# Kernel tuning notes

Measured on AMD Instinct MI355X. Metric: run time of the kernel, lower is better.

The kernel has to match this reference:

```python
import jax, jax.numpy as jnp
import numpy as np

EMBED_DIM = 768
NUM_HEADS = 12
HEAD_DIM = EMBED_DIM // NUM_HEADS
SCALE = HEAD_DIM ** -0.5


def setup_inputs() -> dict:
    key = jax.random.key(0)
    k_x, k_wqkv, k_bqkv, k_wfc, k_bfc = jax.random.split(key, 5)
    B, S, D = 32, 577, EMBED_DIM
    x = jax.random.normal(k_x, (B, S, D), dtype=jnp.float32)
    # torch Linear default init ~ U(-1/sqrt(fan_in), 1/sqrt(fan_in)); scale suffices
    lim = 1.0 / np.sqrt(D)
    w_qkv = jax.random.uniform(k_wqkv, (D, 3 * D), jnp.float32, -lim, lim)
    b_qkv = jax.random.uniform(k_bqkv, (3 * D,), jnp.float32, -lim, lim)
    w_fc = jax.random.uniform(k_wfc, (D, D), jnp.float32, -lim, lim)
    b_fc = jax.random.uniform(k_bfc, (D,), jnp.float32, -lim, lim)
    return {"x": x, "w_qkv": w_qkv, "b_qkv": b_qkv, "w_fc": w_fc, "b_fc": b_fc}


def reference(x, w_qkv, b_qkv, w_fc, b_fc):
    B, S, D = x.shape
    H, Dh = NUM_HEADS, HEAD_DIM
    qkv = x @ w_qkv + b_qkv                      # [B,S,3D]
    qkv = qkv.reshape(B, S, 3, H, Dh)
    q, k, v = jnp.moveaxis(qkv, 2, 0)            # each [B,S,H,Dh]
    # scores: [B,H,S,S]
    attn = jnp.einsum('bqhd,bkhd->bhqk', q, k) * SCALE
    attn = jax.nn.softmax(attn, axis=-1)
    out = jnp.einsum('bhqk,bkhd->bqhd', attn, v).reshape(B, S, D)
    # dropout in eval mode -> identity
    return out @ w_fc + b_fc
```

## Files before the change

### kernel.cpp

```cpp
#include <hip/hip_runtime.h>
#include <hip/hip_bf16.h>
#include <stdint.h>

typedef __attribute__((ext_vector_type(8))) short short8;
typedef __attribute__((ext_vector_type(4))) float f32x4;

typedef __attribute__((address_space(3))) uint8_t lds_u8;
typedef __attribute__((address_space(1))) uint8_t glb_u8;

__device__ __forceinline__ void load_lds_16(const void* g, void* l) {
    __builtin_amdgcn_global_load_lds((glb_u8*)g, (lds_u8*)l, 16, 0, 0);
}

__device__ __forceinline__ unsigned short f2b(float f) {
    __hip_bfloat16 h = __float2bfloat16(f);
    return __builtin_bit_cast(unsigned short, h);
}
__device__ __forceinline__ ushort2 f2b2(float a, float b) {
    __hip_bfloat162 h = __float22bfloat162_rn(float2{a, b});
    ushort2 r;
    __builtin_memcpy(&r, &h, sizeof(r));
    return r;
}

constexpr int Bz = 32, Ss = 577, Dd = 768, Hh = 12;
constexpr int Mm = Bz * Ss;
constexpr int QKV_N = 3 * Dd;
constexpr float SCALE_L2E = 0.125f * 1.4426950408889634f;

__global__ void cast_f32_bf16(const float* __restrict__ src,
                              unsigned short* __restrict__ dst, int n4) {
    int i = blockIdx.x * blockDim.x + threadIdx.x;
    if (i >= n4) return;
    float4 v = ((const float4*)src)[i];
    ushort4 o;
    o.x = f2b(v.x); o.y = f2b(v.y); o.z = f2b(v.z); o.w = f2b(v.w);
    ((ushort4*)dst)[i] = o;
}

__global__ void transpose_cast(const float* __restrict__ src,
                               unsigned short* __restrict__ dst, int R, int C) {
    __shared__ unsigned short tile[32][33];
    int c0 = blockIdx.x * 32, r0 = blockIdx.y * 32;
    int tx = threadIdx.x, ty = threadIdx.y;
#pragma unroll
    for (int i = 0; i < 4; ++i)
        tile[ty + i * 8][tx] = f2b(src[(size_t)(r0 + ty + i * 8) * C + c0 + tx]);
    __syncthreads();
#pragma unroll
    for (int i = 0; i < 4; ++i) {
        int rr = ty + i * 8;
        dst[(size_t)(c0 + rr) * R + r0 + tx] = tile[tx][rr];
    }
}

template <int N_, bool OUT_BF16>
__global__ __launch_bounds__(256)
void gemm_tn(const unsigned short* __restrict__ A,
             const unsigned short* __restrict__ Bt,
             const float* __restrict__ bias,
             void* __restrict__ Cout) {
    constexpr int K = 768;
    constexpr int KB = K / 32;
    constexpr int NX = N_ / 128;
    constexpr int NY = (Mm + 127) / 128;
    constexpr int NWG = NX * NY;
    constexpr int QC = NWG >> 3, RC = NWG & 7;
    __shared__ __align__(16) uint8_t smem[32768];

    const int tid = threadIdx.x;
    const int wave = tid >> 6, lane = tid & 63;
    const int quad = lane >> 4, lc = lane & 15;
    const int wm = wave >> 1, wn = wave & 1;

    const int orig = blockIdx.y * NX + blockIdx.x;
    const int xcd = orig & 7, lid = orig >> 3;
    const int wgid = (xcd < RC ? xcd * (QC + 1) : RC * (QC + 1) + (xcd - RC) * QC) + lid;
    const int tm = (wgid / NX) * 128;
    const int tn = (wgid % NX) * 128;

    const int l4 = lane >> 2;
    const int cx = (lane & 3) ^ (l4 & 3);

    auto stage = [&](int kb, int buf) {
        uint8_t* Ab = smem + buf * 8192;
        uint8_t* Bb = smem + 16384 + buf * 8192;
#pragma unroll
        for (int i = 0; i < 2; ++i) {
            int lrow = wave * 32 + i * 16 + l4;
            int arow = tm + lrow; if (arow >= Mm) arow = Mm - 1;
            load_lds_16(A + (size_t)arow * K + kb * 32 + cx * 8,
                        (void*)(Ab + (wave * 32 + i * 16) * 64));
            int brow = tn + lrow;
            load_lds_16(Bt + (size_t)brow * K + kb * 32 + cx * 8,
                        (void*)(Bb + (wave * 32 + i * 16) * 64));
        }
    };

    f32x4 acc[4][4] = {};
    stage(0, 0);
    __syncthreads();

    for (int kb = 0; kb < KB; ++kb) {
        const int buf = kb & 1;
        if (kb + 1 < KB) stage(kb + 1, buf ^ 1);

        const unsigned short* Ar = (const unsigned short*)(smem + buf * 8192);
        const unsigned short* Br = (const unsigned short*)(smem + 16384 + buf * 8192);
        short8 af[4], bf[4];
#pragma unroll
        for (int i = 0; i < 4; ++i) {
            int row = wm * 64 + i * 16 + lc;
            int c = quad ^ (row & 3);
            af[i] = *(const short8*)(Ar + row * 32 + c * 8);
            int brow = wn * 64 + i * 16 + lc;
            int cb = quad ^ (brow & 3);
            bf[i] = *(const short8*)(Br + brow * 32 + cb * 8);
        }
#pragma unroll
        for (int i = 0; i < 4; ++i)
#pragma unroll
            for (int j = 0; j < 4; ++j)
                acc[i][j] = __builtin_amdgcn_mfma_f32_16x16x32_bf16(af[i], bf[j], acc[i][j], 0, 0, 0);
        __syncthreads();
    }

    float bv[4];
#pragma unroll
    for (int j = 0; j < 4; ++j) bv[j] = bias[tn + wn * 64 + j * 16 + lc];

    float* ep = (float*)smem + wave * (16 * 68);
    const int erow = lane >> 2, ec = (lane & 3) * 16;
#pragma unroll
    for (int i = 0; i < 4; ++i) {
#pragma unroll
        for (int j = 0; j < 4; ++j)
#pragma unroll
            for (int r = 0; r < 4; ++r)
                ep[(quad * 4 + r) * 68 + j * 16 + lc] = acc[i][j][r] + bv[j];
        __threadfence_block();
        int grow = tm + wm * 64 + i * 16 + erow;
        if (grow < Mm) {
            float4 c0 = *(float4*)&ep[erow * 68 + ec + 0];
            float4 c1 = *(float4*)&ep[erow * 68 + ec + 4];
            float4 c2 = *(float4*)&ep[erow * 68 + ec + 8];
            float4 c3 = *(float4*)&ep[erow * 68 + ec + 12];
            int gcol = tn + wn * 64 + ec;
            if constexpr (OUT_BF16) {
                unsigned short o[16];
                *(ushort2*)&o[0]  = f2b2(c0.x, c0.y);
                *(ushort2*)&o[2]  = f2b2(c0.z, c0.w);
                *(ushort2*)&o[4]  = f2b2(c1.x, c1.y);
                *(ushort2*)&o[6]  = f2b2(c1.z, c1.w);
                *(ushort2*)&o[8]  = f2b2(c2.x, c2.y);
                *(ushort2*)&o[10] = f2b2(c2.z, c2.w);
                *(ushort2*)&o[12] = f2b2(c3.x, c3.y);
                *(ushort2*)&o[14] = f2b2(c3.z, c3.w);
                unsigned short* op = (unsigned short*)Cout + (size_t)grow * N_ + gcol;
                *(short8*)(op + 0) = *(short8*)&o[0];
                *(short8*)(op + 8) = *(short8*)&o[8];
            } else {
                float* op = (float*)Cout + (size_t)grow * N_ + gcol;
                *(float4*)(op + 0)  = c0;
                *(float4*)(op + 4)  = c1;
                *(float4*)(op + 8)  = c2;
                *(float4*)(op + 12) = c3;
            }
        }
        __threadfence_block();
    }
}


template <bool TAIL>
__device__ __forceinline__ void attn_tile(
    const unsigned short* __restrict__ Ktile,
    const unsigned short* __restrict__ Vtb,
    unsigned short* __restrict__ Pqw,
    const short8& qf0, const short8& qf1,
    int quad, int lc,
    f32x4 (&oacc)[4], f32x4& lacc) {

    const int sw = lc & 7;
    f32x4 sfr[4];
#pragma unroll
    for (int f = 0; f < 4; ++f) {
        const unsigned short* kr = Ktile + (f * 16 + lc) * 64;
        short8 k0 = *(const short8*)(kr + (quad ^ sw) * 8);
        short8 k1 = *(const short8*)(kr + ((quad ^ 4) ^ sw) * 8);
        f32x4 z = {};
        z = __builtin_amdgcn_mfma_f32_16x16x32_bf16(k0, qf0, z, 0, 0, 0);
        z = __builtin_amdgcn_mfma_f32_16x16x32_bf16(k1, qf1, z, 0, 0, 0);
        sfr[f] = z;
    }

#pragma unroll
    for (int f = 0; f < 4; ++f) {
        float p[4];
#pragma unroll
        for (int r = 0; r < 4; ++r) {
            float s = sfr[f][r];
            if (TAIL && !(f == 0 && r == 0 && quad == 0)) s = -1e30f;
            p[r] = __builtin_amdgcn_exp2f(s * SCALE_L2E);
        }
        ushort2 lo = f2b2(p[0], p[1]), hi = f2b2(p[2], p[3]);
        ushort4 pk = {lo.x, lo.y, hi.x, hi.y};
        *(ushort4*)&Pqw[lc * 72 + f * 16 + quad * 4] = pk;
    }

    __threadfence_block();

    short8 pf0 = *(const short8*)&Pqw[lc * 72 + quad * 8];
    short8 pf1 = *(const short8*)&Pqw[lc * 72 + 32 + quad * 8];
#pragma unroll
    for (int g = 0; g < 4; ++g) {
        short8 vf0 = *(const short8*)&Vtb[(g * 16 + lc) * 80 + quad * 8];
        short8 vf1 = *(const short8*)&Vtb[(g * 16 + lc) * 80 + 32 + quad * 8];
        oacc[g] = __builtin_amdgcn_mfma_f32_16x16x32_bf16(vf0, pf0, oacc[g], 0, 0, 0);
        oacc[g] = __builtin_amdgcn_mfma_f32_16x16x32_bf16(vf1, pf1, oacc[g], 0, 0, 0);
    }
    short8 vo0 = *(const short8*)&Vtb[(64 + lc) * 80 + quad * 8];
    short8 vo1 = *(const short8*)&Vtb[(64 + lc) * 80 + 32 + quad * 8];
    lacc = __builtin_amdgcn_mfma_f32_16x16x32_bf16(vo0, pf0, lacc, 0, 0, 0);
    lacc = __builtin_amdgcn_mfma_f32_16x16x32_bf16(vo1, pf1, lacc, 0, 0, 0);
}

__global__ __launch_bounds__(512)
void attn_kernel(const unsigned short* __restrict__ qkv,
                 unsigned short* __restrict__ outb) {
    __shared__ unsigned short Kt[2][64 * 64];
    __shared__ unsigned short Vt[2][80 * 80];
    __shared__ unsigned short Pq[8][16 * 72];

    const int tid = threadIdx.x;
    const int wave = tid >> 6, lane = tid & 63;
    const int quad = lane >> 4, lc = lane & 15;

    const int orig = (blockIdx.z * gridDim.y + blockIdx.y) * gridDim.x + blockIdx.x;
    const int wgid = (orig & 7) * 240 + (orig >> 3);
    const int qt = wgid % 5;
    const int h  = (wgid / 5) % Hh;
    const int b  = wgid / (5 * Hh);

    const unsigned short* qkvK = qkv + (size_t)b * Ss * QKV_N + h * 64 + 768;
    const unsigned short* qkvV = qkvK + 768;

    const int krow = lane >> 3;
    const int gch = (lane & 7) ^ krow;

    const int qbase = qt * 128 + wave * 16;
    int qrow = qbase + lc; if (qrow > Ss - 1) qrow = Ss - 1;
    const unsigned short* qp = qkv + (size_t)(b * Ss + qrow) * QKV_N + h * 64;
    short8 qf0 = *(const short8*)(qp + quad * 8);
    short8 qf1 = *(const short8*)(qp + 32 + quad * 8);

    unsigned short* Pqw = Pq[wave];

    auto stage_K = [&](int tile, int buf) {
        int key = tile * 64 + wave * 8 + krow; if (key > Ss - 1) key = Ss - 1;
        const unsigned short* gp = qkvK + (size_t)key * QKV_N + gch * 8;
        load_lds_16(gp, (void*)&Kt[buf][wave * 512]);
    };
    auto load_V = [&](int tile) -> short8 {
        int key = tile * 64 + lane; if (key > Ss - 1) key = Ss - 1;
        return *(const short8*)(qkvV + (size_t)key * QKV_N + wave * 8);
    };
    auto write_V = [&](short8 v, int buf) {
#pragma unroll
        for (int j = 0; j < 8; ++j)
            Vt[buf][(wave * 8 + j) * 80 + lane] = (unsigned short)v[j];
    };

    if (tid < 80) {
        Vt[0][64 * 80 + tid] = 0x3F80;
        Vt[1][64 * 80 + tid] = 0x3F80;
    }

    f32x4 oacc[4] = {};
    f32x4 lacc = {};

    stage_K(0, 0);
    write_V(load_V(0), 0);
    __syncthreads();

    for (int kb = 0; kb < 9; ++kb) {
        const int buf = kb & 1;
        stage_K(kb + 1, buf ^ 1);
        short8 vreg = load_V(kb + 1);
        attn_tile<false>(Kt[buf], Vt[buf], Pqw, qf0, qf1, quad, lc, oacc, lacc);
        write_V(vreg, buf ^ 1);
        __syncthreads();
    }
    attn_tile<true>(Kt[1], Vt[1], Pqw, qf0, qf1, quad, lc, oacc, lacc);

    float lq = __shfl(lacc[0], lc, 64);
    float inv = 1.f / lq;
#pragma unroll
    for (int g = 0; g < 4; ++g) {
        ushort2 lo = f2b2(oacc[g][0] * inv, oacc[g][1] * inv);
        ushort2 hi = f2b2(oacc[g][2] * inv, oacc[g][3] * inv);
        ushort4 ob = {lo.x, lo.y, hi.x, hi.y};
        *(ushort4*)&Pqw[lc * 72 + g * 16 + quad * 4] = ob;
    }
    __threadfence_block();
#pragma unroll
    for (int p = 0; p < 2; ++p) {
        int lr = p * 8 + (lane >> 3), ch = lane & 7;
        int q = qbase + lr;
        if (q <= Ss - 1) {
            short8 vv = *(const short8*)&Pqw[lr * 72 + ch * 8];
            *(short8*)(outb + (size_t)(b * Ss + q) * Dd + h * 64 + ch * 8) = vv;
        }
    }
}

extern "C" void kernel_launch(void* const* d_in, const int* in_sizes, int n_in,
                              void* d_out, int out_size, void* d_ws, size_t ws_size,
                              hipStream_t stream) {
    const float* x     = (const float*)d_in[0];
    const float* w_qkv = (const float*)d_in[1];
    const float* b_qkv = (const float*)d_in[2];
    const float* w_fc  = (const float*)d_in[3];
    const float* b_fc  = (const float*)d_in[4];

    uint8_t* ws = (uint8_t*)d_ws;
    unsigned short* xb    = (unsigned short*)(ws + 0);
    unsigned short* wqkvT = (unsigned short*)(ws + 28360704);
    unsigned short* wfcT  = (unsigned short*)(ws + 31899648);
    unsigned short* qkv   = (unsigned short*)(ws + 33079296);
    unsigned short* attn  = (unsigned short*)(ws + 118161408);

    int n4 = (Mm * Dd) / 4;
    cast_f32_bf16<<<(n4 + 255) / 256, 256, 0, stream>>>(x, xb, n4);
    transpose_cast<<<dim3(QKV_N / 32, Dd / 32), dim3(32, 8), 0, stream>>>(w_qkv, wqkvT, Dd, QKV_N);
    transpose_cast<<<dim3(Dd / 32, Dd / 32), dim3(32, 8), 0, stream>>>(w_fc, wfcT, Dd, Dd);

    gemm_tn<QKV_N, true><<<dim3(QKV_N / 128, (Mm + 127) / 128), 256, 0, stream>>>(xb, wqkvT, b_qkv, qkv);

    attn_kernel<<<dim3(5, Hh, Bz), 512, 0, stream>>>(qkv, attn);

    gemm_tn<Dd, false><<<dim3(Dd / 128, (Mm + 127) / 128), 256, 0, stream>>>(attn, wfcT, b_fc, d_out);
}
```

Baseline: 320.6 us.

## Replace 128x128 GEMM with 256x256 eight-wave ping-pong pipelined GEMM

Both projection GEMMs move to a new kernel with 256x256 output tiles, 512 threads and K blocks of 64. It uses 128 KB of dynamic LDS, split into quarter tiles that are staged in a software pipeline two K steps ahead, with `s_setprio` around the MFMA bursts. The aim is more reuse per loaded tile and better overlap of loads with MFMA work. In exchange the grid shrinks a lot: the output projection runs only 219 workgroups, which can leave CUs idle. Occupancy is also limited by the large LDS footprint.

New measurement: 309.2 us. 1.04x faster.

```diff
diff --git a/kernel.cpp b/kernel.cpp
--- a/kernel.cpp
+++ b/kernel.cpp
@@ -55,74 +55,131 @@
 }
 
 template <int N_, bool OUT_BF16>
-__global__ __launch_bounds__(256)
-void gemm_tn(const unsigned short* __restrict__ A,
+__global__ __launch_bounds__(512, 2)
+void gemm256(const unsigned short* __restrict__ A,
              const unsigned short* __restrict__ Bt,
              const float* __restrict__ bias,
              void* __restrict__ Cout) {
     constexpr int K = 768;
-    constexpr int KB = K / 32;
-    constexpr int NX = N_ / 128;
-    constexpr int NY = (Mm + 127) / 128;
+    constexpr int KB = 12;
+    constexpr int NX = N_ / 256;
+    constexpr int NY = (Mm + 255) / 256;
     constexpr int NWG = NX * NY;
     constexpr int QC = NWG >> 3, RC = NWG & 7;
-    __shared__ __align__(16) uint8_t smem[32768];
+    extern __shared__ __align__(16) uint8_t smem[];
 
     const int tid = threadIdx.x;
     const int wave = tid >> 6, lane = tid & 63;
     const int quad = lane >> 4, lc = lane & 15;
-    const int wm = wave >> 1, wn = wave & 1;
+    const int wm = wave >> 2, wn = wave & 3;
 
     const int orig = blockIdx.y * NX + blockIdx.x;
     const int xcd = orig & 7, lid = orig >> 3;
     const int wgid = (xcd < RC ? xcd * (QC + 1) : RC * (QC + 1) + (xcd - RC) * QC) + lid;
-    const int tm = (wgid / NX) * 128;
-    const int tn = (wgid % NX) * 128;
-
-    const int l4 = lane >> 2;
-    const int cx = (lane & 3) ^ (l4 & 3);
-
-    auto stage = [&](int kb, int buf) {
-        uint8_t* Ab = smem + buf * 8192;
-        uint8_t* Bb = smem + 16384 + buf * 8192;
-#pragma unroll
-        for (int i = 0; i < 2; ++i) {
-            int lrow = wave * 32 + i * 16 + l4;
-            int arow = tm + lrow; if (arow >= Mm) arow = Mm - 1;
-            load_lds_16(A + (size_t)arow * K + kb * 32 + cx * 8,
-                        (void*)(Ab + (wave * 32 + i * 16) * 64));
-            int brow = tn + lrow;
-            load_lds_16(Bt + (size_t)brow * K + kb * 32 + cx * 8,
-                        (void*)(Bb + (wave * 32 + i * 16) * 64));
-        }
-    };
-
-    f32x4 acc[4][4] = {};
-    stage(0, 0);
-    __syncthreads();
-
-    for (int kb = 0; kb < KB; ++kb) {
-        const int buf = kb & 1;
-        if (kb + 1 < KB) stage(kb + 1, buf ^ 1);
-
-        const unsigned short* Ar = (const unsigned short*)(smem + buf * 8192);
-        const unsigned short* Br = (const unsigned short*)(smem + 16384 + buf * 8192);
-        short8 af[4], bf[4];
+    const int tm = (wgid / NX) * 256;
+    const int tn = (wgid % NX) * 256;
+
+    const int colsw = ((lane & 7) ^ (lane >> 3)) * 8;
+    const unsigned short* rpA[2][2];
+    const unsigned short* rpB[2][2];
+#pragma unroll
+    for (int s = 0; s < 2; ++s) {
+        const int prs = (s * 8 + wave) * 8 + (lane >> 3);
+#pragma unroll
+        for (int h = 0; h < 2; ++h) {
+            int ar = tm + (prs >> 6) * 128 + h * 64 + (prs & 63);
+            if (ar >= Mm) ar = Mm - 1;
+            rpA[s][h] = A + (size_t)ar * K + colsw;
+            int br = tn + (prs >> 5) * 64 + h * 32 + (prs & 31);
+            rpB[s][h] = Bt + (size_t)br * K + colsw;
+        }
+    }
+
+    auto ldsA = [&](int b, int mh) -> uint8_t* { return smem + b * 65536 + mh * 16384; };
+    auto ldsB = [&](int b, int nh) -> uint8_t* { return smem + b * 65536 + 32768 + nh * 16384; };
+
+    auto stageA = [&](int kb, int mh) {
+        uint8_t* d = ldsA(kb & 1, mh) + wave * 1024;
+        load_lds_16(rpA[0][mh] + kb * 64, d);
+        load_lds_16(rpA[1][mh] + kb * 64, d + 8192);
+    };
+    auto stageB = [&](int kb, int nh) {
+        uint8_t* d = ldsB(kb & 1, nh) + wave * 1024;
+        load_lds_16(rpB[0][nh] + kb * 64, d);
+        load_lds_16(rpB[1][nh] + kb * 64, d + 8192);
+    };
+
+    short8 af[2][4], bf[2][2];
+    auto readA = [&](int b, int mh) {
+        const unsigned short* p = (const unsigned short*)ldsA(b, mh);
 #pragma unroll
         for (int i = 0; i < 4; ++i) {
-            int row = wm * 64 + i * 16 + lc;
-            int c = quad ^ (row & 3);
-            af[i] = *(const short8*)(Ar + row * 32 + c * 8);
-            int brow = wn * 64 + i * 16 + lc;
-            int cb = quad ^ (brow & 3);
-            bf[i] = *(const short8*)(Br + brow * 32 + cb * 8);
-        }
-#pragma unroll
-        for (int i = 0; i < 4; ++i)
-#pragma unroll
-            for (int j = 0; j < 4; ++j)
-                acc[i][j] = __builtin_amdgcn_mfma_f32_16x16x32_bf16(af[i], bf[j], acc[i][j], 0, 0, 0);
-        __syncthreads();
+            const int pr = wm * 64 + i * 16 + lc;
+            const unsigned short* r = p + pr * 64;
+            const int sw = pr & 7;
+            af[0][i] = *(const short8*)(r + ((quad) ^ sw) * 8);
+            af[1][i] = *(const short8*)(r + ((4 + quad) ^ sw) * 8);
+        }
+    };
+    auto readB = [&](int b, int nh) {
+        const unsigned short* p = (const unsigned short*)ldsB(b, nh);
+#pragma unroll
+        for (int j = 0; j < 2; ++j) {
+            const int pr = wn * 32 + j * 16 + lc;
+            const unsigned short* r = p + pr * 64;
+            const int sw = pr & 7;
+            bf[0][j] = *(const short8*)(r + ((quad) ^ sw) * 8);
+            bf[1][j] = *(const short8*)(r + ((4 + quad) ^ sw) * 8);
+        }
+    };
+
+    f32x4 acc[8][4] = {};
+    auto quadmfma = [&](int mh, int nh) {
+        __builtin_amdgcn_s_setprio(1);
+#pragma unroll
+        for (int ks = 0; ks < 2; ++ks)
+#pragma unroll
+            for (int i = 0; i < 4; ++i)
+#pragma unroll
+                for (int j = 0; j < 2; ++j)
+                    acc[mh * 4 + i][nh * 2 + j] = __builtin_amdgcn_mfma_f32_16x16x32_bf16(
+                        af[ks][i], bf[ks][j], acc[mh * 4 + i][nh * 2 + j], 0, 0, 0);
+        __builtin_amdgcn_s_setprio(0);
+    };
+
+    stageA(0, 0); stageB(0, 1); stageA(0, 1); stageB(0, 0);
+    stageA(1, 0); stageB(1, 1);
+    asm volatile("s_waitcnt vmcnt(4)" ::: "memory");
+    __builtin_amdgcn_s_barrier();
+
+    for (int T = 0; T < KB; ++T) {
+        const int rb = T & 1;
+        readA(rb, 0); readB(rb, 0);
+        if (T + 1 < KB) stageA(T + 1, 1);
+        __builtin_amdgcn_s_barrier();
+        asm volatile("s_waitcnt lgkmcnt(0)" ::: "memory");
+        quadmfma(0, 0);
+        __builtin_amdgcn_s_barrier();
+        readB(rb, 1);
+        if (T + 1 < KB) stageB(T + 1, 0);
+        __builtin_amdgcn_s_barrier();
+        asm volatile("s_waitcnt lgkmcnt(0)" ::: "memory");
+        quadmfma(0, 1);
+        __builtin_amdgcn_s_barrier();
+        readA(rb, 1);
+        if (T + 2 < KB) stageA(T + 2, 0);
+        __builtin_amdgcn_s_barrier();
+        asm volatile("s_waitcnt lgkmcnt(0)" ::: "memory");
+        quadmfma(1, 1);
+        __builtin_amdgcn_s_barrier();
+        readB(rb, 0);
+        if (T + 2 < KB) stageB(T + 2, 1);
+        __builtin_amdgcn_s_barrier();
+        asm volatile("s_waitcnt lgkmcnt(0)" ::: "memory");
+        quadmfma(1, 0);
+        if (T + 2 < KB) { asm volatile("s_waitcnt vmcnt(4)" ::: "memory"); }
+        else            { asm volatile("s_waitcnt vmcnt(0)" ::: "memory"); }
+        __builtin_amdgcn_s_barrier();
     }
 
     float bv[4];
@@ -132,14 +189,14 @@
     float* ep = (float*)smem + wave * (16 * 68);
     const int erow = lane >> 2, ec = (lane & 3) * 16;
 #pragma unroll
-    for (int i = 0; i < 4; ++i) {
+    for (int ia = 0; ia < 8; ++ia) {
 #pragma unroll
         for (int j = 0; j < 4; ++j)
 #pragma unroll
             for (int r = 0; r < 4; ++r)
-                ep[(quad * 4 + r) * 68 + j * 16 + lc] = acc[i][j][r] + bv[j];
+                ep[(quad * 4 + r) * 68 + j * 16 + lc] = acc[ia][j][r] + bv[j];
         __threadfence_block();
-        int grow = tm + wm * 64 + i * 16 + erow;
+        int grow = tm + wm * 128 + ia * 16 + erow;
         if (grow < Mm) {
             float4 c0 = *(float4*)&ep[erow * 68 + ec + 0];
             float4 c1 = *(float4*)&ep[erow * 68 + ec + 4];
@@ -171,7 +228,6 @@
     }
 }
 
-
 template <bool TAIL>
 __device__ __forceinline__ void attn_tile(
     const unsigned short* __restrict__ Ktile,
@@ -330,14 +386,23 @@
     unsigned short* qkv   = (unsigned short*)(ws + 33079296);
     unsigned short* attn  = (unsigned short*)(ws + 118161408);
 
+    static bool lds_init = false;
+    if (!lds_init) {
+        hipFuncSetAttribute((const void*)gemm256<QKV_N, true>,
+                            hipFuncAttributeMaxDynamicSharedMemorySize, 131072);
+        hipFuncSetAttribute((const void*)gemm256<Dd, false>,
+                            hipFuncAttributeMaxDynamicSharedMemorySize, 131072);
+        lds_init = true;
+    }
+
     int n4 = (Mm * Dd) / 4;
     cast_f32_bf16<<<(n4 + 255) / 256, 256, 0, stream>>>(x, xb, n4);
     transpose_cast<<<dim3(QKV_N / 32, Dd / 32), dim3(32, 8), 0, stream>>>(w_qkv, wqkvT, Dd, QKV_N);
     transpose_cast<<<dim3(Dd / 32, Dd / 32), dim3(32, 8), 0, stream>>>(w_fc, wfcT, Dd, Dd);
 
-    gemm_tn<QKV_N, true><<<dim3(QKV_N / 128, (Mm + 127) / 128), 256, 0, stream>>>(xb, wqkvT, b_qkv, qkv);
+    gemm256<QKV_N, true><<<dim3(QKV_N / 256, (Mm + 255) / 256), 512, 131072, stream>>>(xb, wqkvT, b_qkv, qkv);
 
     attn_kernel<<<dim3(5, Hh, Bz), 512, 0, stream>>>(qkv, attn);
 
-    gemm_tn<Dd, false><<<dim3(Dd / 128, (Mm + 127) / 128), 256, 0, stream>>>(attn, wfcT, b_fc, d_out);
-}
+    gemm256<Dd, false><<<dim3(Dd / 256, (Mm + 255) / 256), 512, 131072, stream>>>(attn, wfcT, b_fc, d_out);
+}
```

## Replace GEMMs with 256-row two-phase pipelined kernels and add MFMA priority hints

Applied to the files above, without the earlier changes.

Replaces the 128x128 GEMM with a 512-thread kernel covering 256 rows, either 256 or 128 columns per block, using dynamic LDS. The K loop is split into two half-phases, each with its own barriers and explicit vmcnt/lgkmcnt waits, so loads for the next K block overlap with MFMAs on the current one. s_setprio is raised around the MFMA groups in both the GEMM and the attention tile. Bigger tiles give more data reuse per block, but they use more registers and LDS, lower occupancy, and leave fewer blocks in the grid, which can cause tail or load imbalance.

New measurement: 816.6 us. +154.7%, slower.

```diff
diff --git a/kernel.cpp b/kernel.cpp
--- a/kernel.cpp
+++ b/kernel.cpp
@@ -54,123 +54,177 @@
     }
 }
 
-template <int N_, bool OUT_BF16>
-__global__ __launch_bounds__(256)
-void gemm_tn(const unsigned short* __restrict__ A,
+template <int N_, int BN, bool OUT_BF16>
+__global__ __launch_bounds__(512, 4)
+void gemm2ph(const unsigned short* __restrict__ A,
              const unsigned short* __restrict__ Bt,
              const float* __restrict__ bias,
              void* __restrict__ Cout) {
     constexpr int K = 768;
     constexpr int KB = K / 32;
-    constexpr int NX = N_ / 128;
-    constexpr int NY = (Mm + 127) / 128;
+    constexpr int NF = BN / 64;
+    constexpr int NX = N_ / BN;
+    constexpr int NY = (Mm + 255) / 256;
     constexpr int NWG = NX * NY;
     constexpr int QC = NWG >> 3, RC = NWG & 7;
-    __shared__ __align__(16) uint8_t smem[32768];
+    constexpr int ABYTES = 16384;
+    constexpr int BBYTES = BN * 64;
+    constexpr int BUFB = ABYTES + BBYTES;
+    extern __shared__ __align__(16) uint8_t smem[];
 
     const int tid = threadIdx.x;
     const int wave = tid >> 6, lane = tid & 63;
     const int quad = lane >> 4, lc = lane & 15;
-    const int wm = wave >> 1, wn = wave & 1;
+    const int wm = wave >> 2, wn = wave & 3;
 
     const int orig = blockIdx.y * NX + blockIdx.x;
     const int xcd = orig & 7, lid = orig >> 3;
     const int wgid = (xcd < RC ? xcd * (QC + 1) : RC * (QC + 1) + (xcd - RC) * QC) + lid;
-    const int tm = (wgid / NX) * 128;
-    const int tn = (wgid % NX) * 128;
-
-    const int l4 = lane >> 2;
-    const int cx = (lane & 3) ^ (l4 & 3);
-
-    auto stage = [&](int kb, int buf) {
-        uint8_t* Ab = smem + buf * 8192;
-        uint8_t* Bb = smem + 16384 + buf * 8192;
-#pragma unroll
-        for (int i = 0; i < 2; ++i) {
-            int lrow = wave * 32 + i * 16 + l4;
-            int arow = tm + lrow; if (arow >= Mm) arow = Mm - 1;
-            load_lds_16(A + (size_t)arow * K + kb * 32 + cx * 8,
-                        (void*)(Ab + (wave * 32 + i * 16) * 64));
-            int brow = tn + lrow;
-            load_lds_16(Bt + (size_t)brow * K + kb * 32 + cx * 8,
-                        (void*)(Bb + (wave * 32 + i * 16) * 64));
-        }
-    };
-
-    f32x4 acc[4][4] = {};
-    stage(0, 0);
-    __syncthreads();
-
-    for (int kb = 0; kb < KB; ++kb) {
-        const int buf = kb & 1;
-        if (kb + 1 < KB) stage(kb + 1, buf ^ 1);
-
-        const unsigned short* Ar = (const unsigned short*)(smem + buf * 8192);
-        const unsigned short* Br = (const unsigned short*)(smem + 16384 + buf * 8192);
-        short8 af[4], bf[4];
+    const int tm = (wgid / NX) * 256;
+    const int tn = (wgid % NX) * BN;
+
+    const int lr = wave * 16 + (lane >> 2);
+    const int csw = ((lane & 3) ^ ((lane >> 2) & 3)) * 8;
+    const unsigned short* aptr[2];
+    const unsigned short* bptr[2];
+#pragma unroll
+    for (int h = 0; h < 2; ++h) {
+        int ar = tm + (lr & 63) + (lr >> 6) * 128 + h * 64;
+        if (ar >= Mm) ar = Mm - 1;
+        aptr[h] = A + (size_t)ar * K + csw;
+        int br = (BN == 128) ? (tn + lr) : (tn + h * 128 + lr);
+        bptr[h] = Bt + (size_t)br * K + csw;
+    }
+
+    auto stageA = [&](int kb, int h) {
+        load_lds_16(aptr[h] + kb * 32,
+                    smem + (kb & 1) * BUFB + h * 8192 + wave * 1024);
+    };
+    auto stageB = [&](int kb, int h) {
+        load_lds_16(bptr[h] + kb * 32,
+                    smem + (kb & 1) * BUFB + ABYTES + h * 8192 + wave * 1024);
+    };
+
+    short8 af[4], bf[NF];
+    auto readA = [&](int b, int h) {
+        const uint8_t* base = smem + b * BUFB + h * 8192;
 #pragma unroll
         for (int i = 0; i < 4; ++i) {
-            int row = wm * 64 + i * 16 + lc;
-            int c = quad ^ (row & 3);
-            af[i] = *(const short8*)(Ar + row * 32 + c * 8);
-            int brow = wn * 64 + i * 16 + lc;
-            int cb = quad ^ (brow & 3);
-            bf[i] = *(const short8*)(Br + brow * 32 + cb * 8);
-        }
+            int rr = wm * 64 + i * 16 + lc;
+            af[i] = *(const short8*)(base + rr * 64 + ((quad ^ (rr & 3)) << 4));
+        }
+    };
+    auto readB = [&](int b) {
+        const uint8_t* base = smem + b * BUFB + ABYTES;
+#pragma unroll
+        for (int j = 0; j < NF; ++j) {
+            int nr = wn * (BN / 4) + j * 16 + lc;
+            bf[j] = *(const short8*)(base + nr * 64 + ((quad ^ (nr & 3)) << 4));
+        }
+    };
+
+    f32x4 acc[8][NF] = {};
+    auto mfmah = [&](int h) {
+        __builtin_amdgcn_s_setprio(1);
 #pragma unroll
         for (int i = 0; i < 4; ++i)
 #pragma unroll
-            for (int j = 0; j < 4; ++j)
-                acc[i][j] = __builtin_amdgcn_mfma_f32_16x16x32_bf16(af[i], bf[j], acc[i][j], 0, 0, 0);
-        __syncthreads();
-    }
-
-    float bv[4];
-#pragma unroll
-    for (int j = 0; j < 4; ++j) bv[j] = bias[tn + wn * 64 + j * 16 + lc];
-
-    float* ep = (float*)smem + wave * (16 * 68);
-    const int erow = lane >> 2, ec = (lane & 3) * 16;
-#pragma unroll
-    for (int i = 0; i < 4; ++i) {
-#pragma unroll
-        for (int j = 0; j < 4; ++j)
+            for (int j = 0; j < NF; ++j)
+                acc[h * 4 + i][j] = __builtin_amdgcn_mfma_f32_16x16x32_bf16(
+                    af[i], bf[j], acc[h * 4 + i][j], 0, 0, 0);
+        __builtin_amdgcn_s_setprio(0);
+    };
+
+    stageA(0, 0);
+    stageB(0, 0);
+    if (BN == 256) stageB(0, 1);
+    stageA(0, 1);
+    asm volatile("s_waitcnt vmcnt(1)" ::: "memory");
+    __builtin_amdgcn_s_barrier();
+
+    for (int T = 0; T < KB; ++T) {
+        const int rb = T & 1;
+        const bool pf = (T + 1 < KB);
+        readA(rb, 0);
+        readB(rb);
+        if (pf) {
+            stageA(T + 1, 0);
+            stageB(T + 1, 0);
+            if (BN == 256) stageB(T + 1, 1);
+        }
+        __builtin_amdgcn_s_barrier();
+        asm volatile("s_waitcnt lgkmcnt(0)" ::: "memory");
+        mfmah(0);
+        if (pf) {
+            if (BN == 256) asm volatile("s_waitcnt vmcnt(3)" ::: "memory");
+            else           asm volatile("s_waitcnt vmcnt(2)" ::: "memory");
+        } else {
+            asm volatile("s_waitcnt vmcnt(0)" ::: "memory");
+        }
+        __builtin_amdgcn_s_barrier();
+        readA(rb, 1);
+        if (pf) stageA(T + 1, 1);
+        __builtin_amdgcn_s_barrier();
+        asm volatile("s_waitcnt lgkmcnt(0)" ::: "memory");
+        mfmah(1);
+        if (pf) asm volatile("s_waitcnt vmcnt(1)" ::: "memory");
+        __builtin_amdgcn_s_barrier();
+    }
+
+    constexpr int EST = NF * 16 + 4;
+    float bv[NF];
+#pragma unroll
+    for (int j = 0; j < NF; ++j) bv[j] = bias[tn + wn * (BN / 4) + j * 16 + lc];
+
+    float* ep = (float*)smem + wave * (16 * EST);
+    const int erow = lane >> 2, ec = (lane & 3) * (NF * 4);
+#pragma unroll
+    for (int ia = 0; ia < 8; ++ia) {
+#pragma unroll
+        for (int j = 0; j < NF; ++j)
 #pragma unroll
             for (int r = 0; r < 4; ++r)
-                ep[(quad * 4 + r) * 68 + j * 16 + lc] = acc[i][j][r] + bv[j];
+                ep[(quad * 4 + r) * EST + j * 16 + lc] = acc[ia][j][r] + bv[j];
         __threadfence_block();
-        int grow = tm + wm * 64 + i * 16 + erow;
+        int grow = tm + wm * 128 + ia * 16 + erow;
         if (grow < Mm) {
-            float4 c0 = *(float4*)&ep[erow * 68 + ec + 0];
-            float4 c1 = *(float4*)&ep[erow * 68 + ec + 4];
-            float4 c2 = *(float4*)&ep[erow * 68 + ec + 8];
-            float4 c3 = *(float4*)&ep[erow * 68 + ec + 12];
-            int gcol = tn + wn * 64 + ec;
-            if constexpr (OUT_BF16) {
-                unsigned short o[16];
-                *(ushort2*)&o[0]  = f2b2(c0.x, c0.y);
-                *(ushort2*)&o[2]  = f2b2(c0.z, c0.w);
-                *(ushort2*)&o[4]  = f2b2(c1.x, c1.y);
-                *(ushort2*)&o[6]  = f2b2(c1.z, c1.w);
-                *(ushort2*)&o[8]  = f2b2(c2.x, c2.y);
-                *(ushort2*)&o[10] = f2b2(c2.z, c2.w);
-                *(ushort2*)&o[12] = f2b2(c3.x, c3.y);
-                *(ushort2*)&o[14] = f2b2(c3.z, c3.w);
-                unsigned short* op = (unsigned short*)Cout + (size_t)grow * N_ + gcol;
-                *(short8*)(op + 0) = *(short8*)&o[0];
-                *(short8*)(op + 8) = *(short8*)&o[8];
+            int gcol = tn + wn * (BN / 4) + ec;
+            if constexpr (NF == 4) {
+                float4 c0 = *(float4*)&ep[erow * EST + ec + 0];
+                float4 c1 = *(float4*)&ep[erow * EST + ec + 4];
+                float4 c2 = *(float4*)&ep[erow * EST + ec + 8];
+                float4 c3 = *(float4*)&ep[erow * EST + ec + 12];
+                if constexpr (OUT_BF16) {
+                    unsigned short o[16];
+                    *(ushort2*)&o[0]  = f2b2(c0.x, c0.y);
+                    *(ushort2*)&o[2]  = f2b2(c0.z, c0.w);
+                    *(ushort2*)&o[4]  = f2b2(c1.x, c1.y);
+                    *(ushort2*)&o[6]  = f2b2(c1.z, c1.w);
+                    *(ushort2*)&o[8]  = f2b2(c2.x, c2.y);
+                    *(ushort2*)&o[10] = f2b2(c2.z, c2.w);
+                    *(ushort2*)&o[12] = f2b2(c3.x, c3.y);
+                    *(ushort2*)&o[14] = f2b2(c3.z, c3.w);
+                    unsigned short* op = (unsigned short*)Cout + (size_t)grow * N_ + gcol;
+                    *(short8*)(op + 0) = *(short8*)&o[0];
+                    *(short8*)(op + 8) = *(short8*)&o[8];
+                } else {
+                    float* op = (float*)Cout + (size_t)grow * N_ + gcol;
+                    *(float4*)(op + 0)  = c0;
+                    *(float4*)(op + 4)  = c1;
+                    *(float4*)(op + 8)  = c2;
+                    *(float4*)(op + 12) = c3;
+                }
             } else {
+                float4 c0 = *(float4*)&ep[erow * EST + ec + 0];
+                float4 c1 = *(float4*)&ep[erow * EST + ec + 4];
                 float* op = (float*)Cout + (size_t)grow * N_ + gcol;
-                *(float4*)(op + 0)  = c0;
-                *(float4*)(op + 4)  = c1;
-                *(float4*)(op + 8)  = c2;
-                *(float4*)(op + 12) = c3;
+                *(float4*)(op + 0) = c0;
+                *(float4*)(op + 4) = c1;
             }
         }
         __threadfence_block();
     }
 }
-
 
 template <bool TAIL>
 __device__ __forceinline__ void attn_tile(
@@ -183,6 +237,7 @@
 
     const int sw = lc & 7;
     f32x4 sfr[4];
+    __builtin_amdgcn_s_setprio(1);
 #pragma unroll
     for (int f = 0; f < 4; ++f) {
         const unsigned short* kr = Ktile + (f * 16 + lc) * 64;
@@ -193,6 +248,7 @@
         z = __builtin_amdgcn_mfma_f32_16x16x32_bf16(k1, qf1, z, 0, 0, 0);
         sfr[f] = z;
     }
+    __builtin_amdgcn_s_setprio(0);
 
 #pragma unroll
     for (int f = 0; f < 4; ++f) {
@@ -212,6 +268,7 @@
 
     short8 pf0 = *(const short8*)&Pqw[lc * 72 + quad * 8];
     short8 pf1 = *(const short8*)&Pqw[lc * 72 + 32 + quad * 8];
+    __builtin_amdgcn_s_setprio(1);
 #pragma unroll
     for (int g = 0; g < 4; ++g) {
         short8 vf0 = *(const short8*)&Vtb[(g * 16 + lc) * 80 + quad * 8];
@@ -223,6 +280,7 @@
     short8 vo1 = *(const short8*)&Vtb[(64 + lc) * 80 + 32 + quad * 8];
     lacc = __builtin_amdgcn_mfma_f32_16x16x32_bf16(vo0, pf0, lacc, 0, 0, 0);
     lacc = __builtin_amdgcn_mfma_f32_16x16x32_bf16(vo1, pf1, lacc, 0, 0, 0);
+    __builtin_amdgcn_s_setprio(0);
 }
 
 __global__ __launch_bounds__(512)
@@ -330,14 +388,23 @@
     unsigned short* qkv   = (unsigned short*)(ws + 33079296);
     unsigned short* attn  = (unsigned short*)(ws + 118161408);
 
+    static bool lds_init = false;
+    if (!lds_init) {
+        hipFuncSetAttribute((const void*)gemm2ph<QKV_N, 256, true>,
+                            hipFuncAttributeMaxDynamicSharedMemorySize, 65536);
+        hipFuncSetAttribute((const void*)gemm2ph<Dd, 128, false>,
+                            hipFuncAttributeMaxDynamicSharedMemorySize, 49152);
+        lds_init = true;
+    }
+
     int n4 = (Mm * Dd) / 4;
     cast_f32_bf16<<<(n4 + 255) / 256, 256, 0, stream>>>(x, xb, n4);
     transpose_cast<<<dim3(QKV_N / 32, Dd / 32), dim3(32, 8), 0, stream>>>(w_qkv, wqkvT, Dd, QKV_N);
     transpose_cast<<<dim3(Dd / 32, Dd / 32), dim3(32, 8), 0, stream>>>(w_fc, wfcT, Dd, Dd);
 
-    gemm_tn<QKV_N, true><<<dim3(QKV_N / 128, (Mm + 127) / 128), 256, 0, stream>>>(xb, wqkvT, b_qkv, qkv);
+    gemm2ph<QKV_N, 256, true><<<dim3(QKV_N / 256, (Mm + 255) / 256), 512, 65536, stream>>>(xb, wqkvT, b_qkv, qkv);
 
     attn_kernel<<<dim3(5, Hh, Bz), 512, 0, stream>>>(qkv, attn);
 
-    gemm_tn<Dd, false><<<dim3(Dd / 128, (Mm + 127) / 128), 256, 0, stream>>>(attn, wfcT, b_fc, d_out);
-}
+    gemm2ph<Dd, 128, false><<<dim3(Dd / 128, (Mm + 255) / 256), 512, 49152, stream>>>(attn, wfcT, b_fc, d_out);
+}
```
